# Optimization experiments

Hardware: AMD Instinct MI355X
Metric: run time of the kernel (lower is better)

Reference implementation:

```python
import jax, jax.numpy as jnp
import numpy as np

N = 50000      # num nodes
D = 128        # hidden_size
H = 2          # num_head
E = 400000     # num edges / metapath instances
L = 4          # metapath length


def setup_inputs() -> dict:
    key = jax.random.key(0)
    k1, k2, k3, k4, k5, k6 = jax.random.split(key, 6)
    node_features = jax.random.normal(k1, (N, D), dtype=jnp.float32)
    edge_index = jax.random.randint(k2, (2, E), 0, N, dtype=jnp.int64)
    metapath_idx = jax.random.randint(k3, (E, L), 0, N, dtype=jnp.int64)
    s = 1.0 / np.sqrt(D)
    Wq = jax.random.normal(k4, (D, H * D), dtype=jnp.float32) * s
    Wk = jax.random.normal(k5, (D, H * D), dtype=jnp.float32) * s
    Wv = jax.random.normal(k6, (D, H * D), dtype=jnp.float32) * s
    return {"node_features": node_features, "edge_index": edge_index,
            "metapath_idx": metapath_idx, "Wq": Wq, "Wk": Wk, "Wv": Wv}


def _segment_softmax(logits, seg, num_segments):
    # numerically stable softmax over edges grouped by destination node
    m = jax.ops.segment_max(logits, seg, num_segments=num_segments)
    m = jnp.where(jnp.isfinite(m), m, jnp.zeros_like(m))
    ex = jnp.exp(logits - m[seg])
    denom = jax.ops.segment_sum(ex, seg, num_segments=num_segments)
    return ex, denom


def reference(node_features, edge_index, metapath_idx, Wq, Wk, Wv):
    n = node_features.shape[0]
    src, dst = edge_index[0], edge_index[1]

    # --- intra-metapath aggregation (mean over path positions) ---
    metapath_feat = node_features[metapath_idx]          # [E, L, D] gather
    agg = jnp.mean(metapath_feat, axis=1)                # [E, D]
    edge_attr = jnp.broadcast_to(agg[:, None, :], (agg.shape[0], H, D))  # heads tiled -> [E, H, D]

    # --- multi-head edge attention (TransformerConv-style with edge features) ---
    q = (node_features @ Wq).reshape(n, H, D)[dst]       # [E, H, D]
    k = (node_features @ Wk).reshape(n, H, D)[src] + edge_attr
    v = (node_features @ Wv).reshape(n, H, D)[src] + edge_attr

    logits = jnp.einsum('ehd,ehd->eh', q, k) / jnp.sqrt(jnp.float32(D))  # [E, H]
    ex, denom = _segment_softmax(logits, dst, n)
    msg = ex[..., None] * v                              # [E, H, D]
    out = jax.ops.segment_sum(msg, dst, num_segments=n)  # [N, H, D]
    out = out / (denom[..., None] + jnp.float32(1e-16))
    return out.reshape(n, H * D)                         # concat heads -> [N, H*D]
```

## Files before the change

### kernel.cpp

```cpp
#include <hip/hip_runtime.h>
#include <hip/hip_bf16.h>
#include <hip/hip_fp8.h>

#define D_ 128
#define H_ 2
#define L_ 4
#define HD_ 256
#define P2L 0.12751743f

typedef __attribute__((ext_vector_type(8))) short bf16x8;
typedef __attribute__((ext_vector_type(4))) float f32x4;
typedef __attribute__((ext_vector_type(2))) float f32x2;

__device__ __forceinline__ unsigned short f2bf(float x) {
    __hip_bfloat16 b = __float2bfloat16(x);
    return *reinterpret_cast<unsigned short*>(&b);
}
__device__ __forceinline__ float bf2f(unsigned short u) {
    return __uint_as_float(((unsigned)u) << 16);
}
__device__ __forceinline__ unsigned char f2fp8(float x) {
    __hip_fp8_e4m3 t(x);
    return (unsigned char)t.__x;
}
__device__ __forceinline__ float fp82f(unsigned u) {
    __hip_fp8_e4m3 t; t.__x = (__hip_fp8_storage_t)u; return (float)t;
}
__device__ __forceinline__ void unpack_il(const uint4 v, float* h0, float* h1) {
    const unsigned short* u = reinterpret_cast<const unsigned short*>(&v);
#pragma unroll
    for (int j = 0; j < 4; ++j) { h0[j] = bf2f(u[2 * j]); h1[j] = bf2f(u[2 * j + 1]); }
}

#define HIST_BLOCKS 512
__global__ __launch_bounds__(256)
void prep_hist_kernel(const float* __restrict__ nf,
                      const float* __restrict__ Wq, const float* __restrict__ Wk,
                      const float* __restrict__ Wv, const int* __restrict__ dst,
                      unsigned short* __restrict__ nfb, unsigned char* __restrict__ nf8,
                      unsigned short* __restrict__ Wb, int* __restrict__ counts,
                      int n4, int E_) {
    const int nfbB = (n4 + 255) / 256;
    const int bid = blockIdx.x;
    if (bid < nfbB) {
        const int i = bid * 256 + threadIdx.x;
        if (i < n4) {
            const float4 v = reinterpret_cast<const float4*>(nf)[i];
            ushort4 o;
            o.x = f2bf(v.x); o.y = f2bf(v.y); o.z = f2bf(v.z); o.w = f2bf(v.w);
            reinterpret_cast<ushort4*>(nfb)[i] = o;
            const unsigned p8 = (unsigned)f2fp8(v.x) | ((unsigned)f2fp8(v.y) << 8) |
                                ((unsigned)f2fp8(v.z) << 16) | ((unsigned)f2fp8(v.w) << 24);
            reinterpret_cast<unsigned*>(nf8)[i] = p8;
        }
    } else if (bid < nfbB + 384) {
        const int b = bid - nfbB;
        const int n = b * 2 + (threadIdx.x >> 7);
        const int k = threadIdx.x & 127;
        const float* W = (n < 256) ? Wq : (n < 512) ? Wk : Wv;
        const int c = n & 255;
        Wb[(size_t)n * 128 + k] = f2bf(W[(size_t)k * HD_ + c]);
    } else {
        const int b = bid - nfbB - 384;
        const int nquad = E_ >> 2;
        for (int i = b * 256 + threadIdx.x; i < nquad; i += HIST_BLOCKS * 256) {
            const int4 d4 = reinterpret_cast<const int4*>(dst)[i];
            atomicAdd(&counts[d4.x], 1);
            atomicAdd(&counts[d4.y], 1);
            atomicAdd(&counts[d4.z], 1);
            atomicAdd(&counts[d4.w], 1);
        }
        if (b == 0 && (int)threadIdx.x < (E_ & 3))
            atomicAdd(&counts[dst[(E_ & ~3) + threadIdx.x]], 1);
    }
}

__global__ __launch_bounds__(256)
void scan1_kernel(const int* __restrict__ counts, int* __restrict__ offs,
                  int* __restrict__ blksum, int n) {
    __shared__ int sdata[256];
    const int t = threadIdx.x;
    const int base = blockIdx.x * 1024;
    int v[4]; int sum = 0;
#pragma unroll
    for (int j = 0; j < 4; ++j) {
        int idx = base + t * 4 + j;
        v[j] = (idx < n) ? counts[idx] : 0;
        sum += v[j];
    }
    sdata[t] = sum;
    __syncthreads();
    for (int off = 1; off < 256; off <<= 1) {
        int x = (t >= off) ? sdata[t - off] : 0;
        __syncthreads();
        sdata[t] += x;
        __syncthreads();
    }
    if (t == 255) blksum[blockIdx.x] = sdata[255];
    int run = sdata[t] - sum;
#pragma unroll
    for (int j = 0; j < 4; ++j) {
        int idx = base + t * 4 + j;
        if (idx < n) offs[idx] = run;
        run += v[j];
    }
}

__global__ __launch_bounds__(64)
void scan2_kernel(int* __restrict__ blksum, int nblk) {
    const int lane = threadIdx.x;
    int carry = 0;
    for (int base = 0; base < nblk; base += 64) {
        const int idx = base + lane;
        int v = (idx < nblk) ? blksum[idx] : 0;
        int inc = v;
#pragma unroll
        for (int off = 1; off < 64; off <<= 1) {
            int x = __shfl_up(inc, off, 64);
            if (lane >= off) inc += x;
        }
        if (idx < nblk) blksum[idx] = carry + inc - v;
        carry += __shfl(inc, 63, 64);
    }
}

#define SCAT_BLOCKS 1024
__global__ __launch_bounds__(256)
void qkv_scatter_kernel(const unsigned short* __restrict__ nfb,
                        const unsigned short* __restrict__ Wb,
                        unsigned short* __restrict__ Qil,
                        unsigned short* __restrict__ KVil,
                        const int* __restrict__ dst, const int* __restrict__ src,
                        const int* __restrict__ mp, int* __restrict__ offs,
                        const int* __restrict__ blksum,
                        int* __restrict__ srcs, int4* __restrict__ mp4s,
                        int n_nodes, int E_, int qkv_blocks) {
    __shared__ unsigned short sS[32][264];

    if ((int)blockIdx.x >= qkv_blocks) {
        const int b = blockIdx.x - qkv_blocks;
        for (int i = b * 256 + threadIdx.x; i < E_; i += SCAT_BLOCKS * 256) {
            const int d = dst[i];
            const int pos = atomicAdd(&offs[d], 1) + blksum[d >> 10];
            srcs[pos] = src[i];
            mp4s[pos] = *reinterpret_cast<const int4*>(&mp[(size_t)i * L_]);
        }
        return;
    }

    const int tid  = threadIdx.x;
    const int lane = tid & 63;
    const int wv   = tid >> 6;
    const int m0   = blockIdx.x * 32;
    const int r16  = lane & 15;
    const int kg   = lane >> 4;

    bf16x8 afrag[2][4];
#pragma unroll
    for (int ms = 0; ms < 2; ++ms) {
        int arow = m0 + ms * 16 + r16;
        if (arow >= n_nodes) arow = n_nodes - 1;
        const unsigned short* aptr = nfb + (size_t)arow * D_ + kg * 8;
#pragma unroll
        for (int kb = 0; kb < 4; ++kb)
            afrag[ms][kb] = *reinterpret_cast<const bf16x8*>(aptr + kb * 32);
    }

    for (int p = 0; p < 3; ++p) {
#pragma unroll
        for (int j = 0; j < 4; ++j) {
            const int n0 = p * 256 + (wv * 4 + j) * 16;
            const unsigned short* bptr = Wb + (size_t)(n0 + r16) * D_ + kg * 8;
            bf16x8 b0 = *reinterpret_cast<const bf16x8*>(bptr);
            bf16x8 b1 = *reinterpret_cast<const bf16x8*>(bptr + 32);
            bf16x8 b2 = *reinterpret_cast<const bf16x8*>(bptr + 64);
            bf16x8 b3 = *reinterpret_cast<const bf16x8*>(bptr + 96);
            f32x4 acc0 = {0.f, 0.f, 0.f, 0.f};
            f32x4 acc1 = {0.f, 0.f, 0.f, 0.f};
            acc0 = __builtin_amdgcn_mfma_f32_16x16x32_bf16(afrag[0][0], b0, acc0, 0, 0, 0);
            acc1 = __builtin_amdgcn_mfma_f32_16x16x32_bf16(afrag[1][0], b0, acc1, 0, 0, 0);
            acc0 = __builtin_amdgcn_mfma_f32_16x16x32_bf16(afrag[0][1], b1, acc0, 0, 0, 0);
            acc1 = __builtin_amdgcn_mfma_f32_16x16x32_bf16(afrag[1][1], b1, acc1, 0, 0, 0);
            acc0 = __builtin_amdgcn_mfma_f32_16x16x32_bf16(afrag[0][2], b2, acc0, 0, 0, 0);
            acc1 = __builtin_amdgcn_mfma_f32_16x16x32_bf16(afrag[1][2], b2, acc1, 0, 0, 0);
            acc0 = __builtin_amdgcn_mfma_f32_16x16x32_bf16(afrag[0][3], b3, acc0, 0, 0, 0);
            acc1 = __builtin_amdgcn_mfma_f32_16x16x32_bf16(afrag[1][3], b3, acc1, 0, 0, 0);

            const int ln = (n0 & 255) + r16;
            const int il = ((ln & 127) << 1) | ((ln >> 7) & 1);
#pragma unroll
            for (int jj = 0; jj < 4; ++jj) {
                sS[kg * 4 + jj][il]      = f2bf(acc0[jj]);
                sS[16 + kg * 4 + jj][il] = f2bf(acc1[jj]);
            }
        }
        __syncthreads();
        for (int i = tid; i < 32 * 64; i += 256) {
            const int r = i >> 6, c4 = i & 63;
            const int node = m0 + r;
            if (node < n_nodes) {
                const uint2 val = *reinterpret_cast<const uint2*>(&sS[r][c4 * 4]);
                if (p == 0)
                    *reinterpret_cast<uint2*>(&Qil[(size_t)node * HD_ + c4 * 4]) = val;
                else if (p == 1)
                    *reinterpret_cast<uint2*>(&KVil[(size_t)node * 512 + c4 * 4]) = val;
                else
                    *reinterpret_cast<uint2*>(&KVil[(size_t)node * 512 + 256 + c4 * 4]) = val;
            }
        }
        __syncthreads();
    }
}

__global__ __launch_bounds__(128)
void node_fused_kernel(const unsigned char* __restrict__ nf8,
                       const unsigned short* __restrict__ Qil,
                       const unsigned short* __restrict__ KVil,
                       const int* __restrict__ srcs,
                       const int4* __restrict__ mp4s,
                       const int* __restrict__ ends,
                       const int* __restrict__ blksum,
                       const int* __restrict__ counts,
                       float* __restrict__ out,
                       int n_nodes) {
    const int lane = threadIdx.x & 63;
    const int half = lane >> 5;
    const int sl   = lane & 31;
    const int n = __builtin_amdgcn_readfirstlane(
        blockIdx.x * 2 + (threadIdx.x >> 6));
    if (n >= n_nodes) return;

    const int deg = counts[n];
    const int end = ends[n] + blksum[n >> 10];
    const int start = end - deg;
    float* o = out + (size_t)n * HD_;

    if (deg == 0) {
        const float4 z = {0.f, 0.f, 0.f, 0.f};
        *reinterpret_cast<float4*>(&o[half * D_ + sl * 4]) = z;
        return;
    }

    float q0[4], q1[4];
    unpack_il(*reinterpret_cast<const uint4*>(&Qil[(size_t)n * HD_ + sl * 8]), q0, q1);

    float m0 = -INFINITY, m1 = -INFINITY;
    float den0 = 0.f, den1 = 0.f;
    float acc0[4] = {0.f, 0.f, 0.f, 0.f};
    float acc1[4] = {0.f, 0.f, 0.f, 0.f};

#if defined(__has_builtin)
#if __has_builtin(__builtin_amdgcn_cvt_pk_f32_fp8)
#define NFROW(node_id, a)                                                              \
    {                                                                                  \
        const unsigned u = *reinterpret_cast<const unsigned*>(                         \
            &nf8[(size_t)(node_id) * D_ + sl * 4]);                                    \
        const f32x2 lo = __builtin_amdgcn_cvt_pk_f32_fp8((int)u, false);               \
        const f32x2 hi = __builtin_amdgcn_cvt_pk_f32_fp8((int)u, true);                \
        a[0] += lo[0]; a[1] += lo[1]; a[2] += hi[0]; a[3] += hi[1];                    \
    }
#endif
#endif
#ifndef NFROW
#define NFROW(node_id, a)                                                              \
    {                                                                                  \
        const unsigned u = *reinterpret_cast<const unsigned*>(                         \
            &nf8[(size_t)(node_id) * D_ + sl * 4]);                                    \
        a[0] += fp82f(u & 0xffu);         a[1] += fp82f((u >> 8) & 0xffu);             \
        a[2] += fp82f((u >> 16) & 0xffu); a[3] += fp82f((u >> 24) & 0xffu);            \
    }
#endif

#define SMUPDATE(p0, p1, v0, v1, a)                                                    \
    {                                                                                  \
        const float l0 = p0 * P2L, l1 = p1 * P2L;                                      \
        if (l0 > m0 || l1 > m1) {                                                      \
            const float nm0 = fmaxf(m0, l0), nm1 = fmaxf(m1, l1);                      \
            const float c0 = exp2f(m0 - nm0), c1 = exp2f(m1 - nm1);                    \
            den0 *= c0; den1 *= c1;                                                    \
            _Pragma("unroll") for (int j = 0; j < 4; ++j) { acc0[j] *= c0; acc1[j] *= c1; } \
            m0 = nm0; m1 = nm1;                                                        \
        }                                                                              \
        const float e0 = exp2f(l0 - m0), e1 = exp2f(l1 - m1);                          \
        den0 += e0; den1 += e1;                                                        \
        _Pragma("unroll") for (int j = 0; j < 4; ++j) {                                \
            acc0[j] = fmaf(e0, v0[j] + a[j], acc0[j]);                                 \
            acc1[j] = fmaf(e1, v1[j] + a[j], acc1[j]);                                 \
        }                                                                              \
    }

    int i = start + half;
    for (; i + 2 < end; i += 4) {
        const int sA = srcs[i];
        const int sB = srcs[i + 2];
        const int4 mA = mp4s[i];
        const int4 mB = mp4s[i + 2];

        const uint4 kuA = *reinterpret_cast<const uint4*>(&KVil[(size_t)sA * 512 + sl * 8]);
        const uint4 vuA = *reinterpret_cast<const uint4*>(&KVil[(size_t)sA * 512 + 256 + sl * 8]);
        const uint4 kuB = *reinterpret_cast<const uint4*>(&KVil[(size_t)sB * 512 + sl * 8]);
        const uint4 vuB = *reinterpret_cast<const uint4*>(&KVil[(size_t)sB * 512 + 256 + sl * 8]);

        float aA[4] = {0.f, 0.f, 0.f, 0.f};
        float aB[4] = {0.f, 0.f, 0.f, 0.f};
        NFROW(mA.x, aA); NFROW(mA.y, aA); NFROW(mA.z, aA); NFROW(mA.w, aA);
        NFROW(mB.x, aB); NFROW(mB.y, aB); NFROW(mB.z, aB); NFROW(mB.w, aB);
#pragma unroll
        for (int j = 0; j < 4; ++j) { aA[j] *= 0.25f; aB[j] *= 0.25f; }

        float k0A[4], k1A[4], v0A[4], v1A[4];
        float k0B[4], k1B[4], v0B[4], v1B[4];
        unpack_il(kuA, k0A, k1A); unpack_il(vuA, v0A, v1A);
        unpack_il(kuB, k0B, k1B); unpack_il(vuB, v0B, v1B);

        float p0A = 0.f, p1A = 0.f, p0B = 0.f, p1B = 0.f;
#pragma unroll
        for (int j = 0; j < 4; ++j) {
            p0A = fmaf(q0[j], k0A[j] + aA[j], p0A);
            p1A = fmaf(q1[j], k1A[j] + aA[j], p1A);
            p0B = fmaf(q0[j], k0B[j] + aB[j], p0B);
            p1B = fmaf(q1[j], k1B[j] + aB[j], p1B);
        }
#pragma unroll
        for (int off = 1; off < 32; off <<= 1) {
            p0A += __shfl_xor(p0A, off, 64);
            p1A += __shfl_xor(p1A, off, 64);
            p0B += __shfl_xor(p0B, off, 64);
            p1B += __shfl_xor(p1B, off, 64);
        }
        SMUPDATE(p0A, p1A, v0A, v1A, aA);
        SMUPDATE(p0B, p1B, v0B, v1B, aB);
    }
    for (; i < end; i += 2) {
        const int s = srcs[i];
        const int4 mm = mp4s[i];
        const uint4 ku = *reinterpret_cast<const uint4*>(&KVil[(size_t)s * 512 + sl * 8]);
        const uint4 vu = *reinterpret_cast<const uint4*>(&KVil[(size_t)s * 512 + 256 + sl * 8]);
        float a[4] = {0.f, 0.f, 0.f, 0.f};
        NFROW(mm.x, a); NFROW(mm.y, a); NFROW(mm.z, a); NFROW(mm.w, a);
#pragma unroll
        for (int j = 0; j < 4; ++j) a[j] *= 0.25f;
        float k0[4], k1[4], v0[4], v1[4];
        unpack_il(ku, k0, k1); unpack_il(vu, v0, v1);
        float p0 = 0.f, p1 = 0.f;
#pragma unroll
        for (int j = 0; j < 4; ++j) {
            p0 = fmaf(q0[j], k0[j] + a[j], p0);
            p1 = fmaf(q1[j], k1[j] + a[j], p1);
        }
#pragma unroll
        for (int off = 1; off < 32; off <<= 1) {
            p0 += __shfl_xor(p0, off, 64);
            p1 += __shfl_xor(p1, off, 64);
        }
        SMUPDATE(p0, p1, v0, v1, a);
    }

    {
        const float M0 = fmaxf(m0, __shfl_xor(m0, 32, 64));
        const float M1 = fmaxf(m1, __shfl_xor(m1, 32, 64));
        const float c0 = exp2f(m0 - M0), c1 = exp2f(m1 - M1);
        den0 *= c0; den1 *= c1;
#pragma unroll
        for (int j = 0; j < 4; ++j) { acc0[j] *= c0; acc1[j] *= c1; }
        den0 += __shfl_xor(den0, 32, 64);
        den1 += __shfl_xor(den1, 32, 64);
#pragma unroll
        for (int j = 0; j < 4; ++j) {
            acc0[j] += __shfl_xor(acc0[j], 32, 64);
            acc1[j] += __shfl_xor(acc1[j], 32, 64);
        }
    }

    const float r0 = 1.f / (den0 + 1e-16f);
    const float r1 = 1.f / (den1 + 1e-16f);
    float4 ov;
    ov.x = half ? acc1[0] * r1 : acc0[0] * r0;
    ov.y = half ? acc1[1] * r1 : acc0[1] * r0;
    ov.z = half ? acc1[2] * r1 : acc0[2] * r0;
    ov.w = half ? acc1[3] * r1 : acc0[3] * r0;
    *reinterpret_cast<float4*>(&o[half * D_ + sl * 4]) = ov;
#undef NFROW
#undef SMUPDATE
}

extern "C" void kernel_launch(void* const* d_in, const int* in_sizes, int n_in,
                              void* d_out, int out_size, void* d_ws, size_t ws_size,
                              hipStream_t stream) {
    const float* nf  = (const float*)d_in[0];
    const int*   ei  = (const int*)d_in[1];
    const int*   mp  = (const int*)d_in[2];
    const float* Wq  = (const float*)d_in[3];
    const float* Wk  = (const float*)d_in[4];
    const float* Wv  = (const float*)d_in[5];
    float* out = (float*)d_out;

    const int N_nodes = in_sizes[0] / D_;
    const int E_edges = in_sizes[1] / 2;
    const int* src = ei;
    const int* dst = ei + E_edges;

    unsigned short* Qil  = (unsigned short*)d_ws;
    unsigned short* KVil = Qil + (size_t)N_nodes * HD_;
    unsigned short* nfb  = KVil + (size_t)N_nodes * 512;
    unsigned char*  nf8  = (unsigned char*)(nfb + (size_t)N_nodes * D_);
    unsigned short* Wb   = (unsigned short*)(nf8 + (size_t)N_nodes * D_);
    int* counts = (int*)(Wb + (size_t)768 * D_);
    int* offs   = counts + N_nodes;
    int* blksum = offs + N_nodes;
    int* srcs   = blksum + 1024;
    uintptr_t p = (uintptr_t)(srcs + E_edges);
    p = (p + 15) & ~(uintptr_t)15;
    int4* mp4s  = (int4*)p;

    const int nblk1 = (N_nodes + 1023) / 1024;
    const int n4 = N_nodes * D_ / 4;
    const int nfb_blocks = (n4 + 255) / 256;
    const int qkv_blocks = (N_nodes + 31) / 32;

    hipMemsetAsync(counts, 0, (size_t)N_nodes * sizeof(int), stream);

    prep_hist_kernel<<<nfb_blocks + 384 + HIST_BLOCKS, 256, 0, stream>>>(
        nf, Wq, Wk, Wv, dst, nfb, nf8, Wb, counts, n4, E_edges);

    scan1_kernel<<<nblk1, 256, 0, stream>>>(counts, offs, blksum, N_nodes);

    scan2_kernel<<<1, 64, 0, stream>>>(blksum, nblk1);

    qkv_scatter_kernel<<<qkv_blocks + SCAT_BLOCKS, 256, 0, stream>>>(
        nfb, Wb, Qil, KVil, dst, src, mp, offs, blksum, srcs, mp4s,
        N_nodes, E_edges, qkv_blocks);

    node_fused_kernel<<<(N_nodes + 1) / 2, 128, 0, stream>>>(
        nf8, Qil, KVil, srcs, mp4s, offs, blksum, counts, out, N_nodes);
}
```

Baseline: 194.0 us.

## Pack per-edge records, prefetch next records, and widen QKV GEMM row tile

Merges the separate sorted src and metapath arrays into one 32-byte record per edge, so each sorted edge lives in a single cache line. In the node kernel, the records for the next pair of edges are loaded one iteration ahead to hide index-load latency before the dependent K/V and feature gathers. The QKV projection tile grows from 32 to 64 rows per block, so each loaded weight fragment is reused across four MFMA row tiles. In exchange it uses more registers and shared memory, and it writes an extra word per record with padding.

```diff
diff --git a/kernel.cpp b/kernel.cpp
--- a/kernel.cpp
+++ b/kernel.cpp
@@ -125,6 +125,7 @@
 }
 
 #define SCAT_BLOCKS 1024
+#define QROWS 64
 __global__ __launch_bounds__(256)
 void qkv_scatter_kernel(const unsigned short* __restrict__ nfb,
                         const unsigned short* __restrict__ Wb,
@@ -133,17 +134,21 @@
                         const int* __restrict__ dst, const int* __restrict__ src,
                         const int* __restrict__ mp, int* __restrict__ offs,
                         const int* __restrict__ blksum,
-                        int* __restrict__ srcs, int4* __restrict__ mp4s,
+                        int* __restrict__ recs,
                         int n_nodes, int E_, int qkv_blocks) {
-    __shared__ unsigned short sS[32][264];
+    __shared__ unsigned short sS[QROWS][264];
 
     if ((int)blockIdx.x >= qkv_blocks) {
         const int b = blockIdx.x - qkv_blocks;
         for (int i = b * 256 + threadIdx.x; i < E_; i += SCAT_BLOCKS * 256) {
             const int d = dst[i];
             const int pos = atomicAdd(&offs[d], 1) + blksum[d >> 10];
-            srcs[pos] = src[i];
-            mp4s[pos] = *reinterpret_cast<const int4*>(&mp[(size_t)i * L_]);
+            const int4 m4 = *reinterpret_cast<const int4*>(&mp[(size_t)i * L_]);
+            uint4 u0;
+            u0.x = (unsigned)src[i]; u0.y = (unsigned)m4.x;
+            u0.z = (unsigned)m4.y;   u0.w = (unsigned)m4.z;
+            *reinterpret_cast<uint4*>(recs + (size_t)pos * 8) = u0;
+            recs[(size_t)pos * 8 + 4] = m4.w;
         }
         return;
     }
@@ -151,13 +156,13 @@
     const int tid  = threadIdx.x;
     const int lane = tid & 63;
     const int wv   = tid >> 6;
-    const int m0   = blockIdx.x * 32;
+    const int m0   = blockIdx.x * QROWS;
     const int r16  = lane & 15;
     const int kg   = lane >> 4;
 
-    bf16x8 afrag[2][4];
-#pragma unroll
-    for (int ms = 0; ms < 2; ++ms) {
+    bf16x8 afrag[4][4];
+#pragma unroll
+    for (int ms = 0; ms < 4; ++ms) {
         int arow = m0 + ms * 16 + r16;
         if (arow >= n_nodes) arow = n_nodes - 1;
         const unsigned short* aptr = nfb + (size_t)arow * D_ + kg * 8;
@@ -175,28 +180,27 @@
             bf16x8 b1 = *reinterpret_cast<const bf16x8*>(bptr + 32);
             bf16x8 b2 = *reinterpret_cast<const bf16x8*>(bptr + 64);
             bf16x8 b3 = *reinterpret_cast<const bf16x8*>(bptr + 96);
-            f32x4 acc0 = {0.f, 0.f, 0.f, 0.f};
-            f32x4 acc1 = {0.f, 0.f, 0.f, 0.f};
-            acc0 = __builtin_amdgcn_mfma_f32_16x16x32_bf16(afrag[0][0], b0, acc0, 0, 0, 0);
-            acc1 = __builtin_amdgcn_mfma_f32_16x16x32_bf16(afrag[1][0], b0, acc1, 0, 0, 0);
-            acc0 = __builtin_amdgcn_mfma_f32_16x16x32_bf16(afrag[0][1], b1, acc0, 0, 0, 0);
-            acc1 = __builtin_amdgcn_mfma_f32_16x16x32_bf16(afrag[1][1], b1, acc1, 0, 0, 0);
-            acc0 = __builtin_amdgcn_mfma_f32_16x16x32_bf16(afrag[0][2], b2, acc0, 0, 0, 0);
-            acc1 = __builtin_amdgcn_mfma_f32_16x16x32_bf16(afrag[1][2], b2, acc1, 0, 0, 0);
-            acc0 = __builtin_amdgcn_mfma_f32_16x16x32_bf16(afrag[0][3], b3, acc0, 0, 0, 0);
-            acc1 = __builtin_amdgcn_mfma_f32_16x16x32_bf16(afrag[1][3], b3, acc1, 0, 0, 0);
-
+            f32x4 acc[4];
+#pragma unroll
+            for (int ms = 0; ms < 4; ++ms) { acc[ms] = {0.f, 0.f, 0.f, 0.f}; }
+#pragma unroll
+            for (int ms = 0; ms < 4; ++ms) {
+                acc[ms] = __builtin_amdgcn_mfma_f32_16x16x32_bf16(afrag[ms][0], b0, acc[ms], 0, 0, 0);
+                acc[ms] = __builtin_amdgcn_mfma_f32_16x16x32_bf16(afrag[ms][1], b1, acc[ms], 0, 0, 0);
+                acc[ms] = __builtin_amdgcn_mfma_f32_16x16x32_bf16(afrag[ms][2], b2, acc[ms], 0, 0, 0);
+                acc[ms] = __builtin_amdgcn_mfma_f32_16x16x32_bf16(afrag[ms][3], b3, acc[ms], 0, 0, 0);
+            }
             const int ln = (n0 & 255) + r16;
             const int il = ((ln & 127) << 1) | ((ln >> 7) & 1);
 #pragma unroll
-            for (int jj = 0; jj < 4; ++jj) {
-                sS[kg * 4 + jj][il]      = f2bf(acc0[jj]);
-                sS[16 + kg * 4 + jj][il] = f2bf(acc1[jj]);
-            }
+            for (int ms = 0; ms < 4; ++ms)
+#pragma unroll
+                for (int jj = 0; jj < 4; ++jj)
+                    sS[ms * 16 + kg * 4 + jj][il] = f2bf(acc[ms][jj]);
         }
         __syncthreads();
-        for (int i = tid; i < 32 * 64; i += 256) {
-            const int r = i >> 6, c4 = i & 63;
+        for (int i2 = tid; i2 < QROWS * 64; i2 += 256) {
+            const int r = i2 >> 6, c4 = i2 & 63;
             const int node = m0 + r;
             if (node < n_nodes) {
                 const uint2 val = *reinterpret_cast<const uint2*>(&sS[r][c4 * 4]);
@@ -216,8 +220,7 @@
 void node_fused_kernel(const unsigned char* __restrict__ nf8,
                        const unsigned short* __restrict__ Qil,
                        const unsigned short* __restrict__ KVil,
-                       const int* __restrict__ srcs,
-                       const int4* __restrict__ mp4s,
+                       const int* __restrict__ recs,
                        const int* __restrict__ ends,
                        const int* __restrict__ blksum,
                        const int* __restrict__ counts,
@@ -290,11 +293,21 @@
     }
 
     int i = start + half;
-    for (; i + 2 < end; i += 4) {
-        const int sA = srcs[i];
-        const int sB = srcs[i + 2];
-        const int4 mA = mp4s[i];
-        const int4 mB = mp4s[i + 2];
+    uint4 rA = {0, 0, 0, 0}, rB = {0, 0, 0, 0};
+    int wA = 0, wB = 0;
+    if (i < end)     { rA = *reinterpret_cast<const uint4*>(recs + (size_t)i * 8);       wA = recs[(size_t)i * 8 + 4]; }
+    if (i + 2 < end) { rB = *reinterpret_cast<const uint4*>(recs + (size_t)(i + 2) * 8); wB = recs[(size_t)(i + 2) * 8 + 4]; }
+
+    for (; i + 2 < end; ) {
+        const int sA = (int)rA.x, sB = (int)rB.x;
+        const int4 mA = make_int4((int)rA.y, (int)rA.z, (int)rA.w, wA);
+        const int4 mB = make_int4((int)rB.y, (int)rB.z, (int)rB.w, wB);
+
+        const int ni = i + 4;
+        const int pa = (ni < end)     ? ni     : i;
+        const int pb = (ni + 2 < end) ? ni + 2 : i;
+        rA = *reinterpret_cast<const uint4*>(recs + (size_t)pa * 8); wA = recs[(size_t)pa * 8 + 4];
+        rB = *reinterpret_cast<const uint4*>(recs + (size_t)pb * 8); wB = recs[(size_t)pb * 8 + 4];
 
         const uint4 kuA = *reinterpret_cast<const uint4*>(&KVil[(size_t)sA * 512 + sl * 8]);
         const uint4 vuA = *reinterpret_cast<const uint4*>(&KVil[(size_t)sA * 512 + 256 + sl * 8]);
@@ -330,10 +343,13 @@
         }
         SMUPDATE(p0A, p1A, v0A, v1A, aA);
         SMUPDATE(p0B, p1B, v0B, v1B, aB);
+        i = ni;
     }
     for (; i < end; i += 2) {
-        const int s = srcs[i];
-        const int4 mm = mp4s[i];
+        const uint4 r = *reinterpret_cast<const uint4*>(recs + (size_t)i * 8);
+        const int w = recs[(size_t)i * 8 + 4];
+        const int s = (int)r.x;
+        const int4 mm = make_int4((int)r.y, (int)r.z, (int)r.w, w);
         const uint4 ku = *reinterpret_cast<const uint4*>(&KVil[(size_t)s * 512 + sl * 8]);
         const uint4 vu = *reinterpret_cast<const uint4*>(&KVil[(size_t)s * 512 + 256 + sl * 8]);
         float a[4] = {0.f, 0.f, 0.f, 0.f};
@@ -408,15 +424,14 @@
     int* counts = (int*)(Wb + (size_t)768 * D_);
     int* offs   = counts + N_nodes;
     int* blksum = offs + N_nodes;
-    int* srcs   = blksum + 1024;
-    uintptr_t p = (uintptr_t)(srcs + E_edges);
-    p = (p + 15) & ~(uintptr_t)15;
-    int4* mp4s  = (int4*)p;
+    uintptr_t p = (uintptr_t)(blksum + 1024);
+    p = (p + 31) & ~(uintptr_t)31;
+    int* recs   = (int*)p;
 
     const int nblk1 = (N_nodes + 1023) / 1024;
     const int n4 = N_nodes * D_ / 4;
     const int nfb_blocks = (n4 + 255) / 256;
-    const int qkv_blocks = (N_nodes + 31) / 32;
+    const int qkv_blocks = (N_nodes + QROWS - 1) / QROWS;
 
     hipMemsetAsync(counts, 0, (size_t)N_nodes * sizeof(int), stream);
 
@@ -428,9 +443,9 @@
     scan2_kernel<<<1, 64, 0, stream>>>(blksum, nblk1);
 
     qkv_scatter_kernel<<<qkv_blocks + SCAT_BLOCKS, 256, 0, stream>>>(
-        nfb, Wb, Qil, KVil, dst, src, mp, offs, blksum, srcs, mp4s,
+        nfb, Wb, Qil, KVil, dst, src, mp, offs, blksum, recs,
         N_nodes, E_edges, qkv_blocks);
 
     node_fused_kernel<<<(N_nodes + 1) / 2, 128, 0, stream>>>(
-        nf8, Qil, KVil, srcs, mp4s, offs, blksum, counts, out, N_nodes);
-}
+        nf8, Qil, KVil, recs, offs, blksum, counts, out, N_nodes);
+}
```

Result: faster. 176.3 us (-9.2%).
